# Kernel optimization log

Measured on AMD Instinct MI355X. Metric: run time of the kernel, lower is better.

## Reference

```python
import jax, jax.numpy as jnp
import numpy as np
import math

B, C, L_MIX, L_REF = 4, 512, 2048, 2048
NUM_HEADS = 8
HEAD_DIM = C // NUM_HEADS
MAX_LEN = 5000
EPS = 1e-5


def layer_norm(x, gamma, beta):
    mu = jnp.mean(x, axis=-1, keepdims=True)
    var = jnp.mean(jnp.square(x - mu), axis=-1, keepdims=True)
    return (x - mu) * jax.lax.rsqrt(var + EPS) * gamma + beta


def setup_inputs() -> dict:
    key = jax.random.key(0)
    ks = jax.random.split(key, 12)
    inp = {
        "query": jax.random.normal(ks[0], (B, C, L_MIX), dtype=jnp.float32),
        "key_value": jax.random.normal(ks[1], (B, C, L_REF), dtype=jnp.float32),
        "pos_encoding": jax.random.normal(ks[2], (1, MAX_LEN, C), dtype=jnp.float32) * 0.01,
        "q_gamma": jnp.ones((C,), jnp.float32),
        "q_beta": jnp.zeros((C,), jnp.float32),
        "k_gamma": jnp.ones((C,), jnp.float32),
        "k_beta": jnp.zeros((C,), jnp.float32),
        "Wq": jax.random.normal(ks[3], (C, C), jnp.float32) / math.sqrt(C),
        "bq": jax.random.normal(ks[4], (C,), jnp.float32) * 0.01,
        "Wk": jax.random.normal(ks[5], (C, C), jnp.float32) / math.sqrt(C),
        "bk": jax.random.normal(ks[6], (C,), jnp.float32) * 0.01,
        "Wv": jax.random.normal(ks[7], (C, C), jnp.float32) / math.sqrt(C),
        "bv": jax.random.normal(ks[8], (C,), jnp.float32) * 0.01,
        "Wo": jax.random.normal(ks[9], (C, C), jnp.float32) / math.sqrt(C),
        "bo": jax.random.normal(ks[10], (C,), jnp.float32) * 0.01,
    }
    return inp


def reference(query, key_value, pos_encoding, q_gamma, q_beta, k_gamma, k_beta,
              Wq, bq, Wk, bk, Wv, bv, Wo, bo):
    # (B, C, L) -> (B, L, C)
    q = jnp.transpose(query, (0, 2, 1))
    kv = jnp.transpose(key_value, (0, 2, 1))
    Lm, Lr = q.shape[1], kv.shape[1]
    q = q + pos_encoding[:, :Lm, :]
    kv = kv + pos_encoding[:, :Lr, :]
    q = layer_norm(q, q_gamma, q_beta)
    kv = layer_norm(kv, k_gamma, k_beta)
    Q = q @ Wq + bq          # (B, Lm, C)
    K = kv @ Wk + bk         # (B, Lr, C)
    V = kv @ Wv + bv         # (B, Lr, C)
    Q = Q.reshape(B, Lm, NUM_HEADS, HEAD_DIM)
    K = K.reshape(B, Lr, NUM_HEADS, HEAD_DIM)
    V = V.reshape(B, Lr, NUM_HEADS, HEAD_DIM)
    scale = math.sqrt(HEAD_DIM)
    scores = jnp.einsum('bqhd,bkhd->bhqk', Q, K) / scale  # (B, H, Lm, Lr)
    scores = jnp.clip(scores, -50.0, 50.0)
    attn = jax.nn.softmax(scores, axis=-1)  # dropout is identity at eval
    out = jnp.einsum('bhqk,bkhd->bqhd', attn, V).reshape(B, Lm, C)
    out = out @ Wo + bo
    out = out + q            # residual with normed/pos-encoded query, per source
    return jnp.transpose(out, (0, 2, 1))  # (B, C, Lm)
```

## Files before the change

kernel.cpp:

```cpp
#include <hip/hip_runtime.h>
#include <hip/hip_bf16.h>

#define B_ 4
#define C_ 512
#define L_ 2048
#define H_ 8
#define D_ 64
#define EPS_ 1e-5f

using short8 = __attribute__((ext_vector_type(8))) short;
using s4v    = __attribute__((ext_vector_type(4))) short;
using f32x4  = __attribute__((ext_vector_type(4))) float;

#if defined(__has_builtin)
#if __has_builtin(__builtin_amdgcn_exp2f)
#define EXP2(x) __builtin_amdgcn_exp2f(x)
#else
#define EXP2(x) exp2f(x)
#endif
#else
#define EXP2(x) exp2f(x)
#endif

static __device__ __forceinline__ short f2bf(float f) {
  __hip_bfloat16 h = __float2bfloat16(f);
  return __builtin_bit_cast(short, h);
}
static __device__ __forceinline__ float bf2f(short s) {
  return __bfloat162float(__builtin_bit_cast(__hip_bfloat16, s));
}

__global__ __launch_bounds__(256) void k_convert_w(
    const float* __restrict__ Wq, const float* __restrict__ Wk,
    const float* __restrict__ Wv, const float* __restrict__ Wo,
    short* __restrict__ Wt) {
  int m = blockIdx.x, k0 = blockIdx.y * 32, n0 = blockIdx.z * 32;
  const float* W = (m == 0) ? Wq : (m == 1) ? Wk : (m == 2) ? Wv : Wo;
  __shared__ float T[32][33];
  int t = threadIdx.x;
  {
    int kl = t >> 3, n4 = (t & 7) * 4;
    float4 v = *(const float4*)(W + (size_t)(k0 + kl) * C_ + n0 + n4);
    T[kl][n4] = v.x; T[kl][n4 + 1] = v.y; T[kl][n4 + 2] = v.z; T[kl][n4 + 3] = v.w;
  }
  __syncthreads();
  {
    int nl = t >> 3, k4 = (t & 7) * 4;
    s4v o;
#pragma unroll
    for (int j = 0; j < 4; ++j) o[j] = f2bf(T[k4 + j][nl]);
    *(s4v*)(Wt + (size_t)(m * C_ + n0 + nl) * C_ + k0 + k4) = o;
  }
}

__global__ __launch_bounds__(256) void k_prep(
    const float* __restrict__ query, const float* __restrict__ kv,
    const float* __restrict__ pos,
    const float* __restrict__ qg, const float* __restrict__ qb,
    const float* __restrict__ kg, const float* __restrict__ kb,
    short* __restrict__ qn, short* __restrict__ kvn) {
  int l0 = blockIdx.x * 16;
  int b  = blockIdx.y;
  int z  = blockIdx.z;
  const float* src = z ? kv : query;
  const float* g   = z ? kg : qg;
  const float* be  = z ? kb : qb;
  short* dst       = z ? kvn : qn;

  __shared__ float T[16][516];
  __shared__ float mu_s[16], rs_s[16];
  int t = threadIdx.x;

  for (int i = 0; i < 32; ++i) {
    int flat = i * 256 + t;
    int c = flat >> 4, ll = flat & 15;
    T[ll][c] = src[(size_t)(b * C_ + c) * L_ + l0 + ll];
  }
  __syncthreads();
  for (int i = 0; i < 32; ++i) {
    int flat = i * 256 + t;
    int ll = flat >> 9, c = flat & 511;
    T[ll][c] += pos[(size_t)(l0 + ll) * C_ + c];
  }
  __syncthreads();
  {
    int row = t >> 4, j = t & 15;
    float s1 = 0.f, s2 = 0.f;
    for (int c = j; c < C_; c += 16) { float v = T[row][c]; s1 += v; s2 += v * v; }
    for (int m = 1; m < 16; m <<= 1) {
      s1 += __shfl_xor(s1, m, 64);
      s2 += __shfl_xor(s2, m, 64);
    }
    if (j == 0) {
      float mu  = s1 * (1.0f / C_);
      float var = s2 * (1.0f / C_) - mu * mu;
      mu_s[row] = mu;
      rs_s[row] = rsqrtf(var + EPS_);
    }
  }
  __syncthreads();
  for (int i = 0; i < 32; ++i) {
    int flat = i * 256 + t;
    int ll = flat >> 9, c = flat & 511;
    float v = (T[ll][c] - mu_s[ll]) * rs_s[ll] * g[c] + be[c];
    dst[(size_t)(b * L_ + l0 + ll) * C_ + c] = f2bf(v);
  }
}

__global__ __launch_bounds__(256) void k_gemm_qkv(
    const short* __restrict__ qn, const short* __restrict__ kvn,
    const short* __restrict__ Wt,
    const float* __restrict__ bq, const float* __restrict__ bk, const float* __restrict__ bv,
    short* __restrict__ Qw, short* __restrict__ Kw, short* __restrict__ Vw) {
  int z = blockIdx.z;
  const short* X    = z ? kvn : qn;
  const short* W    = Wt + (size_t)z * C_ * C_;
  const float* bias = (z == 0) ? bq : (z == 1) ? bk : bv;
  short* Y          = (z == 0) ? Qw : (z == 1) ? Kw : Vw;
  float sc          = (z == 0) ? 0.18033688f : 1.0f;

  int m0 = blockIdx.x * 128, n0 = blockIdx.y * 128;
  __shared__ alignas(16) short As[128 * 40];
  __shared__ alignas(16) short Bs[128 * 40];
  int t = threadIdx.x, lane = t & 63, w = t >> 6;
  int wm = w & 1, wn = w >> 1;

  f32x4 zero4 = {0.f, 0.f, 0.f, 0.f};
  f32x4 acc[4][4];
  for (int i = 0; i < 4; ++i) for (int j = 0; j < 4; ++j) acc[i][j] = zero4;

  for (int k0 = 0; k0 < C_; k0 += 32) {
    __syncthreads();
    for (int j = 0; j < 2; ++j) {
      int flat = j * 2048 + t * 8;
      int row = flat >> 5, col = flat & 31;
      *(short8*)(As + row * 40 + col) = *(const short8*)(X + (size_t)(m0 + row) * C_ + k0 + col);
      *(short8*)(Bs + row * 40 + col) = *(const short8*)(W + (size_t)(n0 + row) * C_ + k0 + col);
    }
    __syncthreads();
    short8 a[4], bf[4];
    for (int i = 0; i < 4; ++i)
      a[i]  = *(const short8*)(As + (wm * 64 + i * 16 + (lane & 15)) * 40 + ((lane >> 4) << 3));
    for (int i = 0; i < 4; ++i)
      bf[i] = *(const short8*)(Bs + (wn * 64 + i * 16 + (lane & 15)) * 40 + ((lane >> 4) << 3));
    for (int i = 0; i < 4; ++i)
      for (int j = 0; j < 4; ++j)
        acc[i][j] = __builtin_amdgcn_mfma_f32_16x16x32_bf16(a[i], bf[j], acc[i][j], 0, 0, 0);
  }

  for (int i = 0; i < 4; ++i)
    for (int j = 0; j < 4; ++j) {
      int colg = n0 + wn * 64 + j * 16 + (lane & 15);
      float bia = bias[colg];
      for (int r = 0; r < 4; ++r) {
        int rowg = m0 + wm * 64 + i * 16 + (lane >> 4) * 4 + r;
        Y[(size_t)rowg * C_ + colg] = f2bf((acc[i][j][r] + bia) * sc);
      }
    }
}

__global__ __launch_bounds__(256) void k_transpose_v(
    const short* __restrict__ Vw, short* __restrict__ Vtg) {
  int l0 = blockIdx.x * 64, h = blockIdx.y, b = blockIdx.z;
  __shared__ alignas(16) short T[64 * 64];
  int t = threadIdx.x;
#pragma unroll
  for (int p = 0; p < 2; ++p) {
    int flat = p * 256 + t;
    int l = flat >> 3, cc = flat & 7;
    int sw = (l & 7) ^ ((l >> 3) & 7);
    *(short8*)(T + l * 64 + ((cc ^ sw) << 3)) =
        *(const short8*)(Vw + ((size_t)(b * L_ + l0 + l) * H_ + h) * D_ + (cc << 3));
  }
  __syncthreads();
#pragma unroll
  for (int p = 0; p < 2; ++p) {
    int flat = p * 256 + t;
    int d = flat >> 3, l8 = (flat & 7) * 8;
    int sw_hi = (l8 >> 3) & 7;
    short8 o;
#pragma unroll
    for (int j = 0; j < 8; ++j) {
      int pc = (d >> 3) ^ j ^ sw_hi;
      o[j] = T[(l8 + j) * 64 + (pc << 3) + (d & 7)];
    }
    *(short8*)(Vtg + ((size_t)(b * H_ + h) * D_ + d) * L_ + l0 + l8) = o;
  }
}

#define LDP 72
#define LDC 68
__global__ __launch_bounds__(256, 2) void k_attn(
    const short* __restrict__ Qw, const short* __restrict__ Kw,
    const short* __restrict__ Vtg, short* __restrict__ Ow) {
  int l0 = blockIdx.x * 128;
  int h  = blockIdx.y;
  int b  = blockIdx.z;
  __shared__ alignas(16) short Pw[4][16 * LDP];
  __shared__ alignas(16) float Cbuf[128 * LDC];
  __shared__ float Lbuf[128];
  int t = threadIdx.x, lane = t & 63, w = t >> 6;
  int qh = w & 1, ls = w >> 1;
  int quad = lane >> 4, c = lane & 15;

  short8 qa[4][2];
#pragma unroll
  for (int s = 0; s < 4; ++s) {
    const short* qp = Qw + ((size_t)(b * L_ + l0 + qh * 64 + s * 16 + c) * H_ + h) * D_ + quad * 8;
    qa[s][0] = *(const short8*)qp;
    qa[s][1] = *(const short8*)(qp + 32);
  }

  f32x4 zero4 = {0.f, 0.f, 0.f, 0.f};
  f32x4 acc[4][4];
#pragma unroll
  for (int s = 0; s < 4; ++s)
    for (int dt = 0; dt < 4; ++dt) acc[s][dt] = zero4;
  float lsum[4] = {0.f, 0.f, 0.f, 0.f};

  const short* Kb = Kw + ((size_t)(b * L_) * H_ + h) * D_;
  const short* Vb = Vtg + (size_t)(b * H_ + h) * D_ * L_;
  short* pb = &Pw[w][0];

  for (int lr0 = ls * 64; lr0 < L_; lr0 += 128) {
    short8 kf[4][2], vf[4][2];
#pragma unroll
    for (int T = 0; T < 4; ++T) {
      const short* kp = Kb + (size_t)(lr0 + T * 16 + c) * (H_ * D_) + quad * 8;
      kf[T][0] = *(const short8*)kp;
      kf[T][1] = *(const short8*)(kp + 32);
    }
#pragma unroll
    for (int dt = 0; dt < 4; ++dt) {
      const short* vp = Vb + (size_t)(dt * 16 + c) * L_ + lr0 + quad * 8;
      vf[dt][0] = *(const short8*)vp;
      vf[dt][1] = *(const short8*)(vp + 32);
    }

#pragma unroll
    for (int s = 0; s < 4; ++s) {
      f32x4 st[4] = {zero4, zero4, zero4, zero4};
#pragma unroll
      for (int T = 0; T < 4; ++T) {
        st[T] = __builtin_amdgcn_mfma_f32_16x16x32_bf16(kf[T][0], qa[s][0], st[T], 0, 0, 0);
        st[T] = __builtin_amdgcn_mfma_f32_16x16x32_bf16(kf[T][1], qa[s][1], st[T], 0, 0, 0);
      }
#pragma unroll
      for (int T = 0; T < 4; ++T) {
        s4v pk;
#pragma unroll
        for (int r = 0; r < 4; ++r) {
          float p = EXP2(st[T][r]);
          lsum[s] += p;
          pk[r] = f2bf(p);
        }
        *(s4v*)(pb + c * LDP + T * 16 + quad * 4) = pk;
      }
#pragma unroll
      for (int hf = 0; hf < 2; ++hf) {
        short8 pf = *(const short8*)(pb + c * LDP + hf * 32 + quad * 8);
#pragma unroll
        for (int dt = 0; dt < 4; ++dt)
          acc[s][dt] = __builtin_amdgcn_mfma_f32_16x16x32_bf16(vf[dt][hf], pf, acc[s][dt], 0, 0, 0);
      }
    }
  }

#pragma unroll
  for (int s = 0; s < 4; ++s) {
    lsum[s] += __shfl_xor(lsum[s], 16, 64);
    lsum[s] += __shfl_xor(lsum[s], 32, 64);
  }

  if (ls == 1) {
#pragma unroll
    for (int s = 0; s < 4; ++s) {
      int q = qh * 64 + s * 16 + c;
#pragma unroll
      for (int dt = 0; dt < 4; ++dt)
        *(f32x4*)(Cbuf + q * LDC + dt * 16 + quad * 4) = acc[s][dt];
      if (quad == 0) Lbuf[q] = lsum[s];
    }
  }
  __syncthreads();
  if (ls == 0) {
#pragma unroll
    for (int s = 0; s < 4; ++s) {
      int q = qh * 64 + s * 16 + c;
      float inv = 1.0f / (lsum[s] + Lbuf[q]);
#pragma unroll
      for (int dt = 0; dt < 4; ++dt) {
        f32x4 o = *(const f32x4*)(Cbuf + q * LDC + dt * 16 + quad * 4);
        s4v ov;
#pragma unroll
        for (int r = 0; r < 4; ++r) ov[r] = f2bf((acc[s][dt][r] + o[r]) * inv);
        *(s4v*)(Ow + ((size_t)(b * L_ + l0 + q) * H_ + h) * D_ + dt * 16 + quad * 4) = ov;
      }
    }
  }
}

__global__ __launch_bounds__(256) void k_gemm_out(
    const short* __restrict__ Ow, const short* __restrict__ Wot,
    const float* __restrict__ bo, const short* __restrict__ qn,
    float* __restrict__ out) {
  int m0 = blockIdx.x * 128, n0 = blockIdx.y * 128;
  __shared__ alignas(16) short As[128 * 40];
  __shared__ alignas(16) short Bs[128 * 40];
  int t = threadIdx.x, lane = t & 63, w = t >> 6;
  int wm = w & 1, wn = w >> 1;

  f32x4 zero4 = {0.f, 0.f, 0.f, 0.f};
  f32x4 acc[4][4];
  for (int i = 0; i < 4; ++i) for (int j = 0; j < 4; ++j) acc[i][j] = zero4;

  for (int k0 = 0; k0 < C_; k0 += 32) {
    __syncthreads();
    for (int j = 0; j < 2; ++j) {
      int flat = j * 2048 + t * 8;
      int row = flat >> 5, col = flat & 31;
      *(short8*)(As + row * 40 + col) = *(const short8*)(Ow  + (size_t)(m0 + row) * C_ + k0 + col);
      *(short8*)(Bs + row * 40 + col) = *(const short8*)(Wot + (size_t)(n0 + row) * C_ + k0 + col);
    }
    __syncthreads();
    short8 a[4], bf[4];
    for (int i = 0; i < 4; ++i)
      a[i]  = *(const short8*)(As + (wm * 64 + i * 16 + (lane & 15)) * 40 + ((lane >> 4) << 3));
    for (int i = 0; i < 4; ++i)
      bf[i] = *(const short8*)(Bs + (wn * 64 + i * 16 + (lane & 15)) * 40 + ((lane >> 4) << 3));
    for (int i = 0; i < 4; ++i)
      for (int j = 0; j < 4; ++j)
        acc[i][j] = __builtin_amdgcn_mfma_f32_16x16x32_bf16(a[i], bf[j], acc[i][j], 0, 0, 0);
  }

  for (int i = 0; i < 4; ++i)
    for (int j = 0; j < 4; ++j) {
      int colg = n0 + wn * 64 + j * 16 + (lane & 15);
      float bia = bo[colg];
      for (int r = 0; r < 4; ++r) {
        int rowg = m0 + wm * 64 + i * 16 + (lane >> 4) * 4 + r;
        float val = acc[i][j][r] + bia + bf2f(qn[(size_t)rowg * C_ + colg]);
        int bb = rowg >> 11, l = rowg & (L_ - 1);
        out[((size_t)bb * C_ + colg) * L_ + l] = val;
      }
    }
}

extern "C" void kernel_launch(void* const* d_in, const int* in_sizes, int n_in,
                              void* d_out, int out_size, void* d_ws, size_t ws_size,
                              hipStream_t stream) {
  const float* query     = (const float*)d_in[0];
  const float* key_value = (const float*)d_in[1];
  const float* pos       = (const float*)d_in[2];
  const float* qg        = (const float*)d_in[3];
  const float* qb        = (const float*)d_in[4];
  const float* kg        = (const float*)d_in[5];
  const float* kb        = (const float*)d_in[6];
  const float* Wq        = (const float*)d_in[7];
  const float* bq        = (const float*)d_in[8];
  const float* Wk        = (const float*)d_in[9];
  const float* bk        = (const float*)d_in[10];
  const float* Wv        = (const float*)d_in[11];
  const float* bv        = (const float*)d_in[12];
  const float* Wo        = (const float*)d_in[13];
  const float* bo        = (const float*)d_in[14];
  float* out = (float*)d_out;

  char* ws = (char*)d_ws;
  const size_t SZ = (size_t)B_ * L_ * C_ * 2;
  short* qn  = (short*)(ws + 0 * SZ);
  short* kvn = (short*)(ws + 1 * SZ);
  short* Qw  = (short*)(ws + 2 * SZ);
  short* Kw  = (short*)(ws + 3 * SZ);
  short* Vw  = (short*)(ws + 4 * SZ);
  short* Ow  = (short*)(ws + 5 * SZ);
  short* Wt  = (short*)(ws + 6 * SZ);
  short* Vtg = kvn;

  k_convert_w<<<dim3(4, 16, 16), 256, 0, stream>>>(Wq, Wk, Wv, Wo, Wt);
  k_prep<<<dim3(L_ / 16, B_, 2), 256, 0, stream>>>(query, key_value, pos, qg, qb, kg, kb, qn, kvn);
  k_gemm_qkv<<<dim3(8192 / 128, C_ / 128, 3), 256, 0, stream>>>(qn, kvn, Wt, bq, bk, bv, Qw, Kw, Vw);
  k_transpose_v<<<dim3(L_ / 64, H_, B_), 256, 0, stream>>>(Vw, Vtg);
  k_attn<<<dim3(L_ / 128, H_, B_), 256, 0, stream>>>(Qw, Kw, Vtg, Ow);
  k_gemm_out<<<dim3(8192 / 128, C_ / 128, 1), 256, 0, stream>>>(Ow, Wt + (size_t)3 * C_ * C_, bo, qn, out);
}
```

Baseline: 235.5 us.

## Use direct global-to-LDS loads in GEMMs, halve attention query tile, vectorize output stores

Both projection GEMMs now fill shared memory with global_load_lds DMA instead of going through registers, using an unpadded 32-wide LDS layout. The attention kernel processes 64 queries per block instead of 128, giving twice as many blocks, and raises its occupancy hint to 3. The P buffer is now split per query subtile. The output GEMM writes float4 vectors along L. The aim is lower load latency and better GPU fill, at the cost of reloading K and V twice as often in attention and possible LDS bank conflicts from the unpadded layout.

```diff
diff --git a/kernel.cpp b/kernel.cpp
--- a/kernel.cpp
+++ b/kernel.cpp
@@ -21,6 +21,11 @@
 #else
 #define EXP2(x) exp2f(x)
 #endif
+
+#define GLOAD_LDS16(g, l)                                                     \
+  __builtin_amdgcn_global_load_lds(                                           \
+      (const __attribute__((address_space(1))) void*)(g),                     \
+      (__attribute__((address_space(3))) void*)(l), 16, 0, 0)
 
 static __device__ __forceinline__ short f2bf(float f) {
   __hip_bfloat16 h = __float2bfloat16(f);
@@ -120,10 +125,14 @@
   float sc          = (z == 0) ? 0.18033688f : 1.0f;
 
   int m0 = blockIdx.x * 128, n0 = blockIdx.y * 128;
-  __shared__ alignas(16) short As[128 * 40];
-  __shared__ alignas(16) short Bs[128 * 40];
+  __shared__ alignas(16) short As[128 * 32];
+  __shared__ alignas(16) short Bs[128 * 32];
   int t = threadIdx.x, lane = t & 63, w = t >> 6;
   int wm = w & 1, wn = w >> 1;
+  int quad = lane >> 4, c = lane & 15;
+
+  const short* Ag = X + (size_t)(m0 + w * 32 + (lane >> 2)) * C_ + (lane & 3) * 8;
+  const short* Bg = W + (size_t)(n0 + w * 32 + (lane >> 2)) * C_ + (lane & 3) * 8;
 
   f32x4 zero4 = {0.f, 0.f, 0.f, 0.f};
   f32x4 acc[4][4];
@@ -131,31 +140,38 @@
 
   for (int k0 = 0; k0 < C_; k0 += 32) {
     __syncthreads();
+#pragma unroll
     for (int j = 0; j < 2; ++j) {
-      int flat = j * 2048 + t * 8;
-      int row = flat >> 5, col = flat & 31;
-      *(short8*)(As + row * 40 + col) = *(const short8*)(X + (size_t)(m0 + row) * C_ + k0 + col);
-      *(short8*)(Bs + row * 40 + col) = *(const short8*)(W + (size_t)(n0 + row) * C_ + k0 + col);
+      GLOAD_LDS16(Ag + (size_t)j * 16 * C_ + k0, As + (w * 32 + j * 16) * 32);
+      GLOAD_LDS16(Bg + (size_t)j * 16 * C_ + k0, Bs + (w * 32 + j * 16) * 32);
     }
     __syncthreads();
     short8 a[4], bf[4];
-    for (int i = 0; i < 4; ++i)
-      a[i]  = *(const short8*)(As + (wm * 64 + i * 16 + (lane & 15)) * 40 + ((lane >> 4) << 3));
-    for (int i = 0; i < 4; ++i)
-      bf[i] = *(const short8*)(Bs + (wn * 64 + i * 16 + (lane & 15)) * 40 + ((lane >> 4) << 3));
-    for (int i = 0; i < 4; ++i)
+#pragma unroll
+    for (int i = 0; i < 4; ++i)
+      a[i]  = *(const short8*)(As + (wm * 64 + i * 16 + c) * 32 + quad * 8);
+#pragma unroll
+    for (int i = 0; i < 4; ++i)
+      bf[i] = *(const short8*)(Bs + (wn * 64 + i * 16 + c) * 32 + quad * 8);
+#pragma unroll
+    for (int i = 0; i < 4; ++i)
+#pragma unroll
       for (int j = 0; j < 4; ++j)
         acc[i][j] = __builtin_amdgcn_mfma_f32_16x16x32_bf16(a[i], bf[j], acc[i][j], 0, 0, 0);
   }
 
+#pragma unroll
   for (int i = 0; i < 4; ++i)
+#pragma unroll
     for (int j = 0; j < 4; ++j) {
-      int colg = n0 + wn * 64 + j * 16 + (lane & 15);
+      int colg = n0 + wn * 64 + j * 16 + c;
       float bia = bias[colg];
-      for (int r = 0; r < 4; ++r) {
-        int rowg = m0 + wm * 64 + i * 16 + (lane >> 4) * 4 + r;
-        Y[(size_t)rowg * C_ + colg] = f2bf((acc[i][j][r] + bia) * sc);
-      }
+      s4v o;
+#pragma unroll
+      for (int r = 0; r < 4; ++r) o[r] = f2bf((acc[i][j][r] + bia) * sc);
+      int rowg = m0 + wm * 64 + i * 16 + quad * 4;
+#pragma unroll
+      for (int r = 0; r < 4; ++r) Y[(size_t)(rowg + r) * C_ + colg] = o[r];
     }
 }
 
@@ -190,37 +206,36 @@
 
 #define LDP 72
 #define LDC 68
-__global__ __launch_bounds__(256, 2) void k_attn(
+__global__ __launch_bounds__(256, 3) void k_attn(
     const short* __restrict__ Qw, const short* __restrict__ Kw,
     const short* __restrict__ Vtg, short* __restrict__ Ow) {
-  int l0 = blockIdx.x * 128;
+  int l0 = blockIdx.x * 64;
   int h  = blockIdx.y;
   int b  = blockIdx.z;
-  __shared__ alignas(16) short Pw[4][16 * LDP];
-  __shared__ alignas(16) float Cbuf[128 * LDC];
-  __shared__ float Lbuf[128];
+  __shared__ alignas(16) short Pw[4][2][16 * LDP];
+  __shared__ alignas(16) float Cbuf[64 * LDC];
+  __shared__ float Lbuf[64];
   int t = threadIdx.x, lane = t & 63, w = t >> 6;
   int qh = w & 1, ls = w >> 1;
   int quad = lane >> 4, c = lane & 15;
 
-  short8 qa[4][2];
-#pragma unroll
-  for (int s = 0; s < 4; ++s) {
-    const short* qp = Qw + ((size_t)(b * L_ + l0 + qh * 64 + s * 16 + c) * H_ + h) * D_ + quad * 8;
+  short8 qa[2][2];
+#pragma unroll
+  for (int s = 0; s < 2; ++s) {
+    const short* qp = Qw + ((size_t)(b * L_ + l0 + qh * 32 + s * 16 + c) * H_ + h) * D_ + quad * 8;
     qa[s][0] = *(const short8*)qp;
     qa[s][1] = *(const short8*)(qp + 32);
   }
 
   f32x4 zero4 = {0.f, 0.f, 0.f, 0.f};
-  f32x4 acc[4][4];
-#pragma unroll
-  for (int s = 0; s < 4; ++s)
+  f32x4 acc[2][4];
+#pragma unroll
+  for (int s = 0; s < 2; ++s)
     for (int dt = 0; dt < 4; ++dt) acc[s][dt] = zero4;
-  float lsum[4] = {0.f, 0.f, 0.f, 0.f};
+  float lsum[2] = {0.f, 0.f};
 
   const short* Kb = Kw + ((size_t)(b * L_) * H_ + h) * D_;
   const short* Vb = Vtg + (size_t)(b * H_ + h) * D_ * L_;
-  short* pb = &Pw[w][0];
 
   for (int lr0 = ls * 64; lr0 < L_; lr0 += 128) {
     short8 kf[4][2], vf[4][2];
@@ -238,13 +253,14 @@
     }
 
 #pragma unroll
-    for (int s = 0; s < 4; ++s) {
+    for (int s = 0; s < 2; ++s) {
       f32x4 st[4] = {zero4, zero4, zero4, zero4};
 #pragma unroll
       for (int T = 0; T < 4; ++T) {
         st[T] = __builtin_amdgcn_mfma_f32_16x16x32_bf16(kf[T][0], qa[s][0], st[T], 0, 0, 0);
         st[T] = __builtin_amdgcn_mfma_f32_16x16x32_bf16(kf[T][1], qa[s][1], st[T], 0, 0, 0);
       }
+      short* pb = &Pw[w][s][0];
 #pragma unroll
       for (int T = 0; T < 4; ++T) {
         s4v pk;
@@ -267,15 +283,15 @@
   }
 
 #pragma unroll
-  for (int s = 0; s < 4; ++s) {
+  for (int s = 0; s < 2; ++s) {
     lsum[s] += __shfl_xor(lsum[s], 16, 64);
     lsum[s] += __shfl_xor(lsum[s], 32, 64);
   }
 
   if (ls == 1) {
 #pragma unroll
-    for (int s = 0; s < 4; ++s) {
-      int q = qh * 64 + s * 16 + c;
+    for (int s = 0; s < 2; ++s) {
+      int q = qh * 32 + s * 16 + c;
 #pragma unroll
       for (int dt = 0; dt < 4; ++dt)
         *(f32x4*)(Cbuf + q * LDC + dt * 16 + quad * 4) = acc[s][dt];
@@ -285,8 +301,8 @@
   __syncthreads();
   if (ls == 0) {
 #pragma unroll
-    for (int s = 0; s < 4; ++s) {
-      int q = qh * 64 + s * 16 + c;
+    for (int s = 0; s < 2; ++s) {
+      int q = qh * 32 + s * 16 + c;
       float inv = 1.0f / (lsum[s] + Lbuf[q]);
 #pragma unroll
       for (int dt = 0; dt < 4; ++dt) {
@@ -305,10 +321,14 @@
     const float* __restrict__ bo, const short* __restrict__ qn,
     float* __restrict__ out) {
   int m0 = blockIdx.x * 128, n0 = blockIdx.y * 128;
-  __shared__ alignas(16) short As[128 * 40];
-  __shared__ alignas(16) short Bs[128 * 40];
+  __shared__ alignas(16) short As[128 * 32];
+  __shared__ alignas(16) short Bs[128 * 32];
   int t = threadIdx.x, lane = t & 63, w = t >> 6;
   int wm = w & 1, wn = w >> 1;
+  int quad = lane >> 4, c = lane & 15;
+
+  const short* Ag = Ow  + (size_t)(m0 + w * 32 + (lane >> 2)) * C_ + (lane & 3) * 8;
+  const short* Bg = Wot + (size_t)(n0 + w * 32 + (lane >> 2)) * C_ + (lane & 3) * 8;
 
   f32x4 zero4 = {0.f, 0.f, 0.f, 0.f};
   f32x4 acc[4][4];
@@ -316,33 +336,41 @@
 
   for (int k0 = 0; k0 < C_; k0 += 32) {
     __syncthreads();
+#pragma unroll
     for (int j = 0; j < 2; ++j) {
-      int flat = j * 2048 + t * 8;
-      int row = flat >> 5, col = flat & 31;
-      *(short8*)(As + row * 40 + col) = *(const short8*)(Ow  + (size_t)(m0 + row) * C_ + k0 + col);
-      *(short8*)(Bs + row * 40 + col) = *(const short8*)(Wot + (size_t)(n0 + row) * C_ + k0 + col);
+      GLOAD_LDS16(Ag + (size_t)j * 16 * C_ + k0, As + (w * 32 + j * 16) * 32);
+      GLOAD_LDS16(Bg + (size_t)j * 16 * C_ + k0, Bs + (w * 32 + j * 16) * 32);
     }
     __syncthreads();
     short8 a[4], bf[4];
-    for (int i = 0; i < 4; ++i)
-      a[i]  = *(const short8*)(As + (wm * 64 + i * 16 + (lane & 15)) * 40 + ((lane >> 4) << 3));
-    for (int i = 0; i < 4; ++i)
-      bf[i] = *(const short8*)(Bs + (wn * 64 + i * 16 + (lane & 15)) * 40 + ((lane >> 4) << 3));
-    for (int i = 0; i < 4; ++i)
+#pragma unroll
+    for (int i = 0; i < 4; ++i)
+      a[i]  = *(const short8*)(As + (wm * 64 + i * 16 + c) * 32 + quad * 8);
+#pragma unroll
+    for (int i = 0; i < 4; ++i)
+      bf[i] = *(const short8*)(Bs + (wn * 64 + i * 16 + c) * 32 + quad * 8);
+#pragma unroll
+    for (int i = 0; i < 4; ++i)
+#pragma unroll
       for (int j = 0; j < 4; ++j)
         acc[i][j] = __builtin_amdgcn_mfma_f32_16x16x32_bf16(a[i], bf[j], acc[i][j], 0, 0, 0);
   }
 
+  int bb = m0 >> 11;
+#pragma unroll
   for (int i = 0; i < 4; ++i)
+#pragma unroll
     for (int j = 0; j < 4; ++j) {
-      int colg = n0 + wn * 64 + j * 16 + (lane & 15);
+      int colg = n0 + wn * 64 + j * 16 + c;
       float bia = bo[colg];
-      for (int r = 0; r < 4; ++r) {
-        int rowg = m0 + wm * 64 + i * 16 + (lane >> 4) * 4 + r;
-        float val = acc[i][j][r] + bia + bf2f(qn[(size_t)rowg * C_ + colg]);
-        int bb = rowg >> 11, l = rowg & (L_ - 1);
-        out[((size_t)bb * C_ + colg) * L_ + l] = val;
-      }
+      int rowg = m0 + wm * 64 + i * 16 + quad * 4;
+      int l = rowg & (L_ - 1);
+      float4 vv;
+      float* pv = &vv.x;
+#pragma unroll
+      for (int r = 0; r < 4; ++r)
+        pv[r] = acc[i][j][r] + bia + bf2f(qn[(size_t)(rowg + r) * C_ + colg]);
+      *(float4*)(out + ((size_t)bb * C_ + colg) * L_ + l) = vv;
     }
 }
 
@@ -381,6 +409,6 @@
   k_prep<<<dim3(L_ / 16, B_, 2), 256, 0, stream>>>(query, key_value, pos, qg, qb, kg, kb, qn, kvn);
   k_gemm_qkv<<<dim3(8192 / 128, C_ / 128, 3), 256, 0, stream>>>(qn, kvn, Wt, bq, bk, bv, Qw, Kw, Vw);
   k_transpose_v<<<dim3(L_ / 64, H_, B_), 256, 0, stream>>>(Vw, Vtg);
-  k_attn<<<dim3(L_ / 128, H_, B_), 256, 0, stream>>>(Qw, Kw, Vtg, Ow);
+  k_attn<<<dim3(L_ / 64, H_, B_), 256, 0, stream>>>(Qw, Kw, Vtg, Ow);
   k_gemm_out<<<dim3(8192 / 128, C_ / 128, 1), 256, 0, stream>>>(Ow, Wt + (size_t)3 * C_ * C_, bo, qn, out);
 }
```

New measurement: 281.0 us. 19.3% more time.
